# Optimization experiments

Hardware: AMD Instinct MI355X
Metric: run time of the kernel (lower is better)

Reference implementation:

```python
import jax, jax.numpy as jnp
import numpy as np


def setup_inputs() -> dict:
    key = jax.random.key(0)
    k1, k2, k3 = jax.random.split(key, 3)
    B, C, E, L, W = 4, 2, 256, 16000, 40
    mixture_w = jax.random.normal(k1, (B, E, L), dtype=jnp.float32)
    est_mask = jax.random.uniform(k2, (B, C, E, L), dtype=jnp.float32)
    basis_w = jax.random.normal(k3, (W, E), dtype=jnp.float32) * (1.0 / np.sqrt(E))
    return {"mixture_w": mixture_w, "est_mask": est_mask, "basis_w": basis_w}


def overlap_and_add(frames, frame_step):
    # frames: [B, C, L, W] -> [B, C, T] with T = (L-1)*frame_step + W
    B, C, L, W = frames.shape
    T = (L - 1) * frame_step + W
    # scatter-add each frame into the output waveform at its strided offset
    idx = (jnp.arange(L)[:, None] * frame_step + jnp.arange(W)[None, :]).reshape(-1)
    out = jnp.zeros((B, C, T), dtype=frames.dtype)
    return out.at[..., idx].add(frames.reshape(B, C, L * W))


def reference(mixture_w, est_mask, basis_w):
    # mixture_w: [B, E, L], est_mask: [B, C, E, L], basis_w: [W, E]
    source_w = mixture_w[:, None, :, :] * est_mask          # [B, C, E, L]
    # transpose(2,3) then Linear(E->W): contract over E
    est_frames = jnp.einsum('bcel,we->bclw', source_w, basis_w)  # [B, C, L, W]
    W = basis_w.shape[0]
    return overlap_and_add(est_frames, W // 2)              # [B, C, T]
```

## Files before the change

kernel.cpp:

```cpp
#include <hip/hip_runtime.h>

#define BQ   4
#define CQ   2
#define EQ   256
#define LQ   16000
#define WQ   40
#define STEP 20
#define TQ   ((LQ - 1) * STEP + WQ)
#define TLF  63
#define OWN  (TLF * STEP)
#define NBX  254
#define NH   4
#define EH   (EQ / NH)
#define SPAN (TLF * STEP + WQ + STEP)

__global__ void transpose_basis_kernel(const float* __restrict__ basis,
                                       float* __restrict__ wsT) {
    int i = blockIdx.x * 256 + threadIdx.x;
    if (i < EQ * WQ) {
        int e = i / WQ;
        int w = i - e * WQ;
        wsT[i] = basis[w * EQ + e];
    }
}

__global__ __launch_bounds__(512, 8) void decoder_kernel(
    const float* __restrict__ mix,
    const float* __restrict__ mask,
    const float* __restrict__ wsT,
    float* __restrict__ out)
{
    __shared__ float outS[2][CQ][SPAN];

    const int tid = threadIdx.x;
    const int ll  = tid & 63;
    const int c   = (tid >> 6) & 1;
    const int h   = __builtin_amdgcn_readfirstlane(tid >> 7);
    const int bx  = blockIdx.x;
    const int b   = blockIdx.y;
    const int f   = TLF * bx - 1 + ll;

    const int   fc    = min(max(f, 0), LQ - 1);
    const float valid = (f >= 0 && f < LQ) ? 1.0f : 0.0f;

    float acc[WQ];
#pragma unroll
    for (int w = 0; w < WQ; ++w) acc[w] = 0.0f;

    const float* mp = mix  + ((size_t)b * EQ + h * EH) * LQ + fc;
    const float* kp = mask + (((size_t)(b * CQ + c)) * EQ + h * EH) * LQ + fc;
    const float* bp = wsT + (size_t)h * EH * WQ;

    for (int eo = 0; eo < EH; eo += 2) {
        float m0 = mp[(size_t)eo * LQ];
        float m1 = mp[(size_t)(eo + 1) * LQ];
        float k0 = kp[(size_t)eo * LQ] * valid;
        float k1 = kp[(size_t)(eo + 1) * LQ] * valid;
        {
            float s = m0 * k0;
            const float* bb = bp + eo * WQ;
#pragma unroll
            for (int w = 0; w < WQ; ++w) acc[w] = fmaf(s, bb[w], acc[w]);
        }
        {
            float s = m1 * k1;
            const float* bb = bp + (eo + 1) * WQ;
#pragma unroll
            for (int w = 0; w < WQ; ++w) acc[w] = fmaf(s, bb[w], acc[w]);
        }
    }

    const int base = ll * STEP;
    const int cp   = h >> 1;
    const int hp   = h & 1;
    if (hp == 0 && (ll & 1) == 0) {
#pragma unroll
        for (int w = 0; w < WQ; ++w) outS[cp][c][base + w] = acc[w];
    }
    __syncthreads();
    if (hp == 0 && (ll & 1) == 1) {
#pragma unroll
        for (int w = 0; w < WQ; ++w) outS[cp][c][base + w] += acc[w];
    }
    __syncthreads();
    if (hp == 1 && (ll & 1) == 0) {
#pragma unroll
        for (int w = 0; w < WQ; ++w) outS[cp][c][base + w] += acc[w];
    }
    __syncthreads();
    if (hp == 1 && (ll & 1) == 1) {
#pragma unroll
        for (int w = 0; w < WQ; ++w) outS[cp][c][base + w] += acc[w];
    }
    __syncthreads();

    for (int cc = 0; cc < CQ; ++cc) {
        const size_t ob = ((size_t)b * CQ + cc) * TQ + (size_t)OWN * bx;
        for (int i = tid; i < OWN; i += 512) {
            const long t = (long)OWN * bx + i;
            if (t < (long)TQ) {
                out[ob + i] = outS[0][cc][STEP + i] + outS[1][cc][STEP + i];
            }
        }
    }
}

extern "C" void kernel_launch(void* const* d_in, const int* in_sizes, int n_in,
                              void* d_out, int out_size, void* d_ws, size_t ws_size,
                              hipStream_t stream) {
    const float* mix   = (const float*)d_in[0];
    const float* mask  = (const float*)d_in[1];
    const float* basis = (const float*)d_in[2];
    float* out = (float*)d_out;
    float* wsT = (float*)d_ws;

    transpose_basis_kernel<<<dim3((EQ * WQ + 255) / 256), 256, 0, stream>>>(basis, wsT);

    dim3 grid(NBX, BQ);
    decoder_kernel<<<grid, 512, 0, stream>>>(mix, mask, wsT, out);
}
```

Before: 241.1 us.

## Compute both channels per thread to share mixture loads, split E across eight wave groups

Each thread now accumulates both mask channels, so every mixture value and basis coefficient it loads feeds two accumulator sets. The reduction dimension E is split into eight slices instead of four, with four shared-memory partial buffers summed at write-out. This halves redundant mixture and basis reads, but doubles accumulator registers (80 floats), lowers the occupancy hint to 4 and increases LDS usage per block.

```diff
diff --git a/kernel.cpp b/kernel.cpp
--- a/kernel.cpp
+++ b/kernel.cpp
@@ -10,8 +10,9 @@
 #define TLF  63
 #define OWN  (TLF * STEP)
 #define NBX  254
-#define NH   4
+#define NH   8
 #define EH   (EQ / NH)
+#define NCP  4
 #define SPAN (TLF * STEP + WQ + STEP)
 
 __global__ void transpose_basis_kernel(const float* __restrict__ basis,
@@ -24,18 +25,17 @@
     }
 }
 
-__global__ __launch_bounds__(512, 8) void decoder_kernel(
+__global__ __launch_bounds__(512, 4) void decoder_kernel(
     const float* __restrict__ mix,
     const float* __restrict__ mask,
     const float* __restrict__ wsT,
     float* __restrict__ out)
 {
-    __shared__ float outS[2][CQ][SPAN];
+    __shared__ float outS[NCP][CQ][SPAN];
 
     const int tid = threadIdx.x;
     const int ll  = tid & 63;
-    const int c   = (tid >> 6) & 1;
-    const int h   = __builtin_amdgcn_readfirstlane(tid >> 7);
+    const int h   = __builtin_amdgcn_readfirstlane(tid >> 6);
     const int bx  = blockIdx.x;
     const int b   = blockIdx.y;
     const int f   = TLF * bx - 1 + ll;
@@ -43,30 +43,41 @@
     const int   fc    = min(max(f, 0), LQ - 1);
     const float valid = (f >= 0 && f < LQ) ? 1.0f : 0.0f;
 
-    float acc[WQ];
+    float acc0[WQ], acc1[WQ];
 #pragma unroll
-    for (int w = 0; w < WQ; ++w) acc[w] = 0.0f;
+    for (int w = 0; w < WQ; ++w) { acc0[w] = 0.0f; acc1[w] = 0.0f; }
 
-    const float* mp = mix  + ((size_t)b * EQ + h * EH) * LQ + fc;
-    const float* kp = mask + (((size_t)(b * CQ + c)) * EQ + h * EH) * LQ + fc;
-    const float* bp = wsT + (size_t)h * EH * WQ;
+    const float* mp  = mix  + ((size_t)b * EQ + h * EH) * LQ + fc;
+    const float* kp0 = mask + (((size_t)(b * CQ)) * EQ + h * EH) * LQ + fc;
+    const float* kp1 = kp0 + (size_t)EQ * LQ;
+    const float* bp  = wsT + (size_t)h * EH * WQ;
 
     for (int eo = 0; eo < EH; eo += 2) {
-        float m0 = mp[(size_t)eo * LQ];
-        float m1 = mp[(size_t)(eo + 1) * LQ];
-        float k0 = kp[(size_t)eo * LQ] * valid;
-        float k1 = kp[(size_t)(eo + 1) * LQ] * valid;
+        float m0  = mp[(size_t)eo * LQ];
+        float m1  = mp[(size_t)(eo + 1) * LQ];
+        float k00 = kp0[(size_t)eo * LQ] * valid;
+        float k01 = kp0[(size_t)(eo + 1) * LQ] * valid;
+        float k10 = kp1[(size_t)eo * LQ] * valid;
+        float k11 = kp1[(size_t)(eo + 1) * LQ] * valid;
         {
-            float s = m0 * k0;
+            float s0 = m0 * k00;
+            float s1 = m0 * k10;
             const float* bb = bp + eo * WQ;
 #pragma unroll
-            for (int w = 0; w < WQ; ++w) acc[w] = fmaf(s, bb[w], acc[w]);
+            for (int w = 0; w < WQ; ++w) {
+                acc0[w] = fmaf(s0, bb[w], acc0[w]);
+                acc1[w] = fmaf(s1, bb[w], acc1[w]);
+            }
         }
         {
-            float s = m1 * k1;
+            float s0 = m1 * k01;
+            float s1 = m1 * k11;
             const float* bb = bp + (eo + 1) * WQ;
 #pragma unroll
-            for (int w = 0; w < WQ; ++w) acc[w] = fmaf(s, bb[w], acc[w]);
+            for (int w = 0; w < WQ; ++w) {
+                acc0[w] = fmaf(s0, bb[w], acc0[w]);
+                acc1[w] = fmaf(s1, bb[w], acc1[w]);
+            }
         }
     }
 
@@ -75,22 +86,34 @@
     const int hp   = h & 1;
     if (hp == 0 && (ll & 1) == 0) {
 #pragma unroll
-        for (int w = 0; w < WQ; ++w) outS[cp][c][base + w] = acc[w];
+        for (int w = 0; w < WQ; ++w) {
+            outS[cp][0][base + w] = acc0[w];
+            outS[cp][1][base + w] = acc1[w];
+        }
     }
     __syncthreads();
     if (hp == 0 && (ll & 1) == 1) {
 #pragma unroll
-        for (int w = 0; w < WQ; ++w) outS[cp][c][base + w] += acc[w];
+        for (int w = 0; w < WQ; ++w) {
+            outS[cp][0][base + w] += acc0[w];
+            outS[cp][1][base + w] += acc1[w];
+        }
     }
     __syncthreads();
     if (hp == 1 && (ll & 1) == 0) {
 #pragma unroll
-        for (int w = 0; w < WQ; ++w) outS[cp][c][base + w] += acc[w];
+        for (int w = 0; w < WQ; ++w) {
+            outS[cp][0][base + w] += acc0[w];
+            outS[cp][1][base + w] += acc1[w];
+        }
     }
     __syncthreads();
     if (hp == 1 && (ll & 1) == 1) {
 #pragma unroll
-        for (int w = 0; w < WQ; ++w) outS[cp][c][base + w] += acc[w];
+        for (int w = 0; w < WQ; ++w) {
+            outS[cp][0][base + w] += acc0[w];
+            outS[cp][1][base + w] += acc1[w];
+        }
     }
     __syncthreads();
 
@@ -99,7 +122,8 @@
         for (int i = tid; i < OWN; i += 512) {
             const long t = (long)OWN * bx + i;
             if (t < (long)TQ) {
-                out[ob + i] = outS[0][cc][STEP + i] + outS[1][cc][STEP + i];
+                out[ob + i] = outS[0][cc][STEP + i] + outS[1][cc][STEP + i]
+                            + outS[2][cc][STEP + i] + outS[3][cc][STEP + i];
             }
         }
     }
```

After: 244.5 us. About the same (+1.4%).
